# Kernel optimization log

Measured on AMD Instinct MI355X. Metric: run time of the kernel, lower is better.

## Reference

```python
import jax, jax.numpy as jnp
import numpy as np

L, H, C, HS, V, BS = 4, 8, 512, 64, 32000, 2048  # layers, heads, n_embd, head_size, vocab, block_size
B, T = 2, 2048


def _ln(x, g, b, eps=1e-5):
    m = jnp.mean(x, axis=-1, keepdims=True)
    v = jnp.var(x, axis=-1, keepdims=True)
    return (x - m) * jax.lax.rsqrt(v + eps) * g + b


def setup_inputs() -> dict:
    key = jax.random.key(0)
    ks = jax.random.split(key, 12)
    s = 0.02
    f = jnp.float32
    return {
        "idx": jax.random.randint(ks[0], (B, T), 0, V),
        "tok_emb": jax.random.normal(ks[1], (V, C), f) * s,
        "pos_emb": jax.random.normal(ks[2], (BS, C), f) * s,
        "ln1_g": jnp.ones((L, C), f), "ln1_b": jnp.zeros((L, C), f),
        "wq": jax.random.normal(ks[3], (L, H, C, HS), f) * s,
        "wk": jax.random.normal(ks[4], (L, H, C, HS), f) * s,
        "wv": jax.random.normal(ks[5], (L, H, C, HS), f) * s,
        "proj_w": jax.random.normal(ks[6], (L, C, C), f) * s,
        "proj_b": jnp.zeros((L, C), f),
        "ln2_g": jnp.ones((L, C), f), "ln2_b": jnp.zeros((L, C), f),
        "ff_w1": jax.random.normal(ks[7], (L, C, 4 * C), f) * s,
        "ff_b1": jnp.zeros((L, 4 * C), f),
        "ff_w2": jax.random.normal(ks[8], (L, 4 * C, C), f) * s,
        "ff_b2": jnp.zeros((L, C), f),
        "ffln_g": jnp.ones((L, C), f), "ffln_b": jnp.zeros((L, C), f),
        "lm_w": jax.random.normal(ks[9], (C, V), f) * s,
        "lm_b": jnp.zeros((V,), f),
    }


def reference(idx, tok_emb, pos_emb, ln1_g, ln1_b, wq, wk, wv, proj_w, proj_b,
              ln2_g, ln2_b, ff_w1, ff_b1, ff_w2, ff_b2, ffln_g, ffln_b, lm_w, lm_b):
    Tn = idx.shape[1]
    x = tok_emb[idx] + pos_emb[:Tn]  # [B,T,C]
    causal = jnp.tril(jnp.ones((Tn, Tn), bool))
    for l in range(L):
        h = _ln(x, ln1_g[l], ln1_b[l])
        q = jnp.einsum('btc,hcd->bhtd', h, wq[l])
        k = jnp.einsum('btc,hcd->bhtd', h, wk[l])
        v = jnp.einsum('btc,hcd->bhtd', h, wv[l])
        # NOTE: original module does NOT scale by 1/sqrt(head_size)
        wei = jnp.einsum('bhtd,bhsd->bhts', q, k)
        wei = jnp.where(causal, wei, -jnp.inf)
        wei = jax.nn.softmax(wei, axis=-1)
        att = jnp.einsum('bhts,bhsd->bhtd', wei, v)  # [B,H,T,HS]
        att = att.transpose(0, 2, 1, 3).reshape(x.shape[0], Tn, C)
        x = x + att @ proj_w[l].T + proj_b[l]
        h2 = _ln(x, ln2_g[l], ln2_b[l])
        ff = jax.nn.relu(h2 @ ff_w1[l] + ff_b1[l]) @ ff_w2[l] + ff_b2[l]
        ff = _ln(ff, ffln_g[l], ffln_b[l])  # FeedForward has trailing LayerNorm
        x = x + ff
    logits = x @ lm_w + lm_b  # [B,T,V]
    return logits
```

## Files before the change

### kernel.cpp

```cpp
#include <hip/hip_runtime.h>
#include <math.h>

#define NLAYER 4
#define NH     8
#define CDIM   512
#define HS     64
#define VOCAB  32000
#define BB     2
#define TT     2048
#define MROWS  (BB*TT)
#define QKVW   (3*CDIM)
#define NHEADS (BB*NH)
#define ASPLIT 2

typedef __attribute__((ext_vector_type(8))) short bf16x8;
typedef __attribute__((ext_vector_type(4))) float f32x4;

__device__ __forceinline__ unsigned short f2bf(float f) {
    unsigned int u = __float_as_uint(f);
    u += 0x7FFF + ((u >> 16) & 1);
    return (unsigned short)(u >> 16);
}

#define GLOAD16(g, l) __builtin_amdgcn_global_load_lds( \
    (const __attribute__((address_space(1))) void*)(g), \
    (__attribute__((address_space(3))) void*)(l), 16, 0, 0)

#define SWZ(row, chunk) (((row)*64) + ((((chunk) ^ ((row)&7)))*8))

template<int FLAGS, bool OUTBF, bool MSWIZ>
__global__ __launch_bounds__(256) void mfma_gemm(
    const unsigned short* __restrict__ A, int lda,
    const unsigned short* __restrict__ Bt, int ldb,
    const float* __restrict__ bias,
    void* __restrict__ Cout, int ldc,
    const float* __restrict__ resid,
    int K)
{
    __shared__ unsigned short As[2][128*64];
    __shared__ unsigned short Bs[2][128*64];
    const int tid = threadIdx.x;
    const int w = tid >> 6, l = tid & 63;
    const int wr = w >> 1, wc = w & 1;
    long m0, n0;
    if (MSWIZ) {
        const int mt = gridDim.x;
        const int flat = blockIdx.y * mt + blockIdx.x;
        const int cpx = (mt * gridDim.y) >> 3;
        const int swz = (flat & 7) * cpx + (flat >> 3);
        m0 = (long)(swz % mt) * 128;
        n0 = (long)(swz / mt) * 128;
    } else {
        m0 = (long)blockIdx.y * 128;
        n0 = (long)blockIdx.x * 128;
    }
    const int srow = l >> 3;
    const int scol = ((l & 7) ^ (srow & 7)) << 3;
    const unsigned short* Ab = A + m0*lda;
    const unsigned short* Bb = Bt + n0*ldb;
    const int fr = l & 15;
    const int g  = l >> 4;

    f32x4 acc[4][4];
    #pragma unroll
    for (int m = 0; m < 4; m++)
        #pragma unroll
        for (int n = 0; n < 4; n++) acc[m][n] = (f32x4)0.0f;

    auto stage = [&](int k0, int buf) {
        #pragma unroll
        for (int i = 0; i < 4; i++) {
            int seg = w*4 + i;
            GLOAD16(Ab + (long)(seg*8 + srow)*lda + k0 + scol, &As[buf][seg*512]);
            GLOAD16(Bb + (long)(seg*8 + srow)*ldb + k0 + scol, &Bs[buf][seg*512]);
        }
    };

    const int nk = K >> 6;
    stage(0, 0);
    for (int ks = 0; ks < nk; ks++) {
        const int buf = ks & 1;
        __syncthreads();
        if (ks + 1 < nk) stage((ks+1) << 6, buf ^ 1);
        #pragma unroll
        for (int kk = 0; kk < 2; kk++) {
            bf16x8 af[4], bf[4];
            #pragma unroll
            for (int m = 0; m < 4; m++) {
                int row = wr*64 + m*16 + fr;
                af[m] = *(const bf16x8*)&As[buf][SWZ(row, kk*4 + g)];
            }
            #pragma unroll
            for (int n = 0; n < 4; n++) {
                int row = wc*64 + n*16 + fr;
                bf[n] = *(const bf16x8*)&Bs[buf][SWZ(row, kk*4 + g)];
            }
            #pragma unroll
            for (int m = 0; m < 4; m++)
                #pragma unroll
                for (int n = 0; n < 4; n++)
                    acc[m][n] = __builtin_amdgcn_mfma_f32_16x16x32_bf16(
                        af[m], bf[n], acc[m][n], 0, 0, 0);
        }
    }

    const int rg = g << 2;
    #pragma unroll
    for (int n = 0; n < 4; n++) {
        long gn = n0 + wc*64 + n*16 + fr;
        float bv = (FLAGS & 1) ? bias[gn] : 0.f;
        #pragma unroll
        for (int m = 0; m < 4; m++) {
            #pragma unroll
            for (int r = 0; r < 4; r++) {
                long gm = m0 + wr*64 + m*16 + rg + r;
                float val = acc[m][n][r] + bv;
                if (FLAGS & 2) val = fmaxf(val, 0.f);
                if (FLAGS & 4) val += resid[gm*ldc + gn];
                if (OUTBF) {
                    ((unsigned short*)Cout)[gm*ldc + gn] = f2bf(val);
                } else if (FLAGS & 8) {
                    __builtin_nontemporal_store(val, &((float*)Cout)[gm*ldc + gn]);
                } else {
                    ((float*)Cout)[gm*ldc + gn] = val;
                }
            }
        }
    }
}

__global__ __launch_bounds__(256) void mfma_gemm_pk(
    const unsigned short* __restrict__ A, int lda,
    const unsigned short* __restrict__ Bt, int ldb,
    float* __restrict__ part, int ldc, long zstride,
    int Kc)
{
    __shared__ unsigned short As[2][128*64];
    __shared__ unsigned short Bs[2][128*64];
    const int tid = threadIdx.x;
    const int w = tid >> 6, l = tid & 63;
    const int wr = w >> 1, wc = w & 1;
    const long m0 = (long)blockIdx.y * 128;
    const long n0 = (long)blockIdx.x * 128;
    const int z = blockIdx.z;
    const int srow = l >> 3;
    const int scol = ((l & 7) ^ (srow & 7)) << 3;
    const unsigned short* Ab = A + m0*lda + (long)z*Kc;
    const unsigned short* Bb = Bt + n0*ldb + (long)z*Kc;
    float* Cb = part + (long)z*zstride;
    const int fr = l & 15;
    const int g  = l >> 4;

    f32x4 acc[4][4];
    #pragma unroll
    for (int m = 0; m < 4; m++)
        #pragma unroll
        for (int n = 0; n < 4; n++) acc[m][n] = (f32x4)0.0f;

    auto stage = [&](int k0, int buf) {
        #pragma unroll
        for (int i = 0; i < 4; i++) {
            int seg = w*4 + i;
            GLOAD16(Ab + (long)(seg*8 + srow)*lda + k0 + scol, &As[buf][seg*512]);
            GLOAD16(Bb + (long)(seg*8 + srow)*ldb + k0 + scol, &Bs[buf][seg*512]);
        }
    };

    const int nk = Kc >> 6;
    stage(0, 0);
    for (int ks = 0; ks < nk; ks++) {
        const int buf = ks & 1;
        __syncthreads();
        if (ks + 1 < nk) stage((ks+1) << 6, buf ^ 1);
        #pragma unroll
        for (int kk = 0; kk < 2; kk++) {
            bf16x8 af[4], bf[4];
            #pragma unroll
            for (int m = 0; m < 4; m++) {
                int row = wr*64 + m*16 + fr;
                af[m] = *(const bf16x8*)&As[buf][SWZ(row, kk*4 + g)];
            }
            #pragma unroll
            for (int n = 0; n < 4; n++) {
                int row = wc*64 + n*16 + fr;
                bf[n] = *(const bf16x8*)&Bs[buf][SWZ(row, kk*4 + g)];
            }
            #pragma unroll
            for (int m = 0; m < 4; m++)
                #pragma unroll
                for (int n = 0; n < 4; n++)
                    acc[m][n] = __builtin_amdgcn_mfma_f32_16x16x32_bf16(
                        af[m], bf[n], acc[m][n], 0, 0, 0);
        }
    }

    const int rg = g << 2;
    #pragma unroll
    for (int n = 0; n < 4; n++) {
        long gn = n0 + wc*64 + n*16 + fr;
        #pragma unroll
        for (int m = 0; m < 4; m++)
            #pragma unroll
            for (int r = 0; r < 4; r++) {
                long gm = m0 + wr*64 + m*16 + rg + r;
                Cb[gm*ldc + gn] = acc[m][n][r];
            }
    }
}

template<int NS, int RESID>
__global__ __launch_bounds__(256) void reduce_add(
    const float* __restrict__ part, const float* __restrict__ bias,
    float* __restrict__ out)
{
    const long i4 = ((long)blockIdx.x*256 + threadIdx.x) * 4;
    float4 s = *(const float4*)(bias + (i4 & (CDIM-1)));
    #pragma unroll
    for (int z = 0; z < NS; z++) {
        float4 p = *(const float4*)(part + (long)z*MROWS*CDIM + i4);
        s.x += p.x; s.y += p.y; s.z += p.z; s.w += p.w;
    }
    float4* o = (float4*)(out + i4);
    if (RESID) {
        float4 old = *o;
        s.x += old.x; s.y += old.y; s.z += old.z; s.w += old.w;
    }
    *o = s;
}

__global__ __launch_bounds__(256) void mfma_gemm_qkv(
    const unsigned short* __restrict__ A,
    const unsigned short* __restrict__ Bt,
    unsigned short* __restrict__ qh,
    unsigned short* __restrict__ kh,
    unsigned short* __restrict__ vt)
{
    __shared__ unsigned short As[2][128*64];
    __shared__ unsigned short Bs[2][128*64];
    const int tid = threadIdx.x;
    const int w = tid >> 6, l = tid & 63;
    const int wr = w >> 1, wc = w & 1;
    const long m0 = (long)blockIdx.y * 128;
    const long n0 = (long)blockIdx.x * 128;
    const int srow = l >> 3;
    const int scol = ((l & 7) ^ (srow & 7)) << 3;
    const unsigned short* Ab = A + m0*CDIM;
    const unsigned short* Bb = Bt + n0*CDIM;
    const int fr = l & 15;
    const int g  = l >> 4;

    f32x4 acc[4][4];
    #pragma unroll
    for (int m = 0; m < 4; m++)
        #pragma unroll
        for (int n = 0; n < 4; n++) acc[m][n] = (f32x4)0.0f;

    auto stage = [&](int k0, int buf) {
        #pragma unroll
        for (int i = 0; i < 4; i++) {
            int seg = w*4 + i;
            GLOAD16(Ab + (long)(seg*8 + srow)*CDIM + k0 + scol, &As[buf][seg*512]);
            GLOAD16(Bb + (long)(seg*8 + srow)*CDIM + k0 + scol, &Bs[buf][seg*512]);
        }
    };

    const int nk = CDIM >> 6;
    stage(0, 0);
    for (int ks = 0; ks < nk; ks++) {
        const int buf = ks & 1;
        __syncthreads();
        if (ks + 1 < nk) stage((ks+1) << 6, buf ^ 1);
        #pragma unroll
        for (int kk = 0; kk < 2; kk++) {
            bf16x8 af[4], bf[4];
            #pragma unroll
            for (int m = 0; m < 4; m++) {
                int row = wr*64 + m*16 + fr;
                af[m] = *(const bf16x8*)&As[buf][SWZ(row, kk*4 + g)];
            }
            #pragma unroll
            for (int n = 0; n < 4; n++) {
                int row = wc*64 + n*16 + fr;
                bf[n] = *(const bf16x8*)&Bs[buf][SWZ(row, kk*4 + g)];
            }
            #pragma unroll
            for (int m = 0; m < 4; m++)
                #pragma unroll
                for (int n = 0; n < 4; n++)
                    acc[m][n] = __builtin_amdgcn_mfma_f32_16x16x32_bf16(
                        af[m], bf[n], acc[m][n], 0, 0, 0);
        }
    }

    const int rg = g << 2;
    #pragma unroll
    for (int n = 0; n < 4; n++) {
        int gn = (int)(n0 + wc*64 + n*16 + fr);
        int which = gn >> 9, hh = (gn >> 6) & 7, d = gn & 63;
        #pragma unroll
        for (int m = 0; m < 4; m++) {
            #pragma unroll
            for (int r = 0; r < 4; r++) {
                int gm = (int)(m0 + wr*64 + m*16 + rg + r);
                int b = gm >> 11, t = gm & (TT-1);
                int head = b*NH + hh;
                unsigned short val = f2bf(acc[m][n][r]);
                if (which == 0)      qh[((long)head*TT + t)*HS + d] = val;
                else if (which == 1) kh[((long)head*TT + t)*HS + d] = val;
                else                 vt[((long)head*HS + d)*TT + t] = val;
            }
        }
    }
}

__global__ __launch_bounds__(256) void attn_part(
    const unsigned short* __restrict__ qh,
    const unsigned short* __restrict__ kh,
    const unsigned short* __restrict__ vt,
    float* __restrict__ oP, float* __restrict__ ml)
{
    __shared__ unsigned short Ks[2][64*64];
    __shared__ unsigned short Vts[2][64*64];
    __shared__ unsigned short Ps[4][32*72];
    const int tid = threadIdx.x;
    const int w = tid >> 6, l = tid & 63;
    const int fr = l & 15, g = l >> 4;
    const int head = blockIdx.y;
    const int sp = blockIdx.z;
    const int x = blockIdx.x;
    const int qw = x*128 + w*32;
    const unsigned short* Qb = qh + (long)head*TT*HS;
    const unsigned short* Kb = kh + (long)head*TT*HS;
    const unsigned short* Vb = vt + (long)head*HS*TT;

    bf16x8 aq[2][2];
    #pragma unroll
    for (int mt = 0; mt < 2; mt++)
        #pragma unroll
        for (int ks = 0; ks < 2; ks++)
            aq[mt][ks] = *(const bf16x8*)&Qb[(long)(qw + mt*16 + fr)*HS + ks*32 + g*8];

    f32x4 acc_o[2][4];
    float mrun[2][4], lsum[2][4];
    #pragma unroll
    for (int mt = 0; mt < 2; mt++) {
        #pragma unroll
        for (int r = 0; r < 4; r++) { mrun[mt][r] = -INFINITY; lsum[mt][r] = 0.f; }
        #pragma unroll
        for (int n = 0; n < 4; n++) acc_o[mt][n] = (f32x4)0.0f;
    }

    const int nch = 2*x + 2;
    const int qq = nch / ASPLIT, rr = nch % ASPLIT;
    const int cbeg = sp*qq + (sp < rr ? sp : rr);
    const int cend = cbeg + qq + (sp < rr ? 1 : 0);
    const int srow = l >> 3;
    const int scol = ((l & 7) ^ (srow & 7)) << 3;

    auto stage = [&](int c) {
        int buf = c & 1;
        int s0_ = c*64;
        #pragma unroll
        for (int i = 0; i < 2; i++) {
            int rb = i*32 + w*8;
            GLOAD16(Kb + (long)(s0_ + rb + srow)*HS + scol, &Ks[buf][rb*64]);
            GLOAD16(Vb + (long)(rb + srow)*TT + s0_ + scol, &Vts[buf][rb*64]);
        }
    };

    if (cbeg < cend) stage(cbeg);
    for (int c = cbeg; c < cend; c++) {
        const int s0 = c*64;
        const int buf = c & 1;
        __syncthreads();
        if (c + 1 < cend) stage(c+1);
        if (s0 > qw + 31) continue;

        bf16x8 bk[4][2];
        #pragma unroll
        for (int n = 0; n < 4; n++)
            #pragma unroll
            for (int ks = 0; ks < 2; ks++) {
                int row = n*16 + fr;
                bk[n][ks] = *(const bf16x8*)&Ks[buf][SWZ(row, ks*4 + g)];
            }
        f32x4 sc[2][4];
        #pragma unroll
        for (int mt = 0; mt < 2; mt++)
            #pragma unroll
            for (int n = 0; n < 4; n++) sc[mt][n] = (f32x4)0.0f;
        #pragma unroll
        for (int ks = 0; ks < 2; ks++)
            #pragma unroll
            for (int mt = 0; mt < 2; mt++)
                #pragma unroll
                for (int n = 0; n < 4; n++)
                    sc[mt][n] = __builtin_amdgcn_mfma_f32_16x16x32_bf16(
                        aq[mt][ks], bk[n][ks], sc[mt][n], 0, 0, 0);

        #pragma unroll
        for (int mt = 0; mt < 2; mt++) {
            #pragma unroll
            for (int r = 0; r < 4; r++) {
                int q = qw + mt*16 + g*4 + r;
                float rmax = -INFINITY;
                #pragma unroll
                for (int n = 0; n < 4; n++) {
                    float v = sc[mt][n][r];
                    v = (s0 + n*16 + fr <= q) ? v : -INFINITY;
                    sc[mt][n][r] = v;
                    rmax = fmaxf(rmax, v);
                }
                #pragma unroll
                for (int off = 8; off >= 1; off >>= 1)
                    rmax = fmaxf(rmax, __shfl_xor(rmax, off));
                float mnew = fmaxf(mrun[mt][r], rmax);
                float scale = __expf(mrun[mt][r] - mnew);
                float ps = 0.f;
                #pragma unroll
                for (int n = 0; n < 4; n++) {
                    float p = __expf(sc[mt][n][r] - mnew);
                    sc[mt][n][r] = p;
                    ps += p;
                }
                #pragma unroll
                for (int off = 8; off >= 1; off >>= 1)
                    ps += __shfl_xor(ps, off);
                lsum[mt][r] = lsum[mt][r]*scale + ps;
                mrun[mt][r] = mnew;
                #pragma unroll
                for (int n = 0; n < 4; n++) acc_o[mt][n][r] *= scale;
            }
        }

        #pragma unroll
        for (int mt = 0; mt < 2; mt++)
            #pragma unroll
            for (int n = 0; n < 4; n++)
                #pragma unroll
                for (int r = 0; r < 4; r++)
                    Ps[w][(mt*16 + g*4 + r)*72 + n*16 + fr] = f2bf(sc[mt][n][r]);

        bf16x8 ap[2][2], bv[4][2];
        #pragma unroll
        for (int mt = 0; mt < 2; mt++)
            #pragma unroll
            for (int ks = 0; ks < 2; ks++)
                ap[mt][ks] = *(const bf16x8*)&Ps[w][(mt*16 + fr)*72 + ks*32 + g*8];
        #pragma unroll
        for (int n = 0; n < 4; n++)
            #pragma unroll
            for (int ks = 0; ks < 2; ks++) {
                int row = n*16 + fr;
                bv[n][ks] = *(const bf16x8*)&Vts[buf][SWZ(row, ks*4 + g)];
            }
        #pragma unroll
        for (int ks = 0; ks < 2; ks++)
            #pragma unroll
            for (int mt = 0; mt < 2; mt++)
                #pragma unroll
                for (int n = 0; n < 4; n++)
                    acc_o[mt][n] = __builtin_amdgcn_mfma_f32_16x16x32_bf16(
                        ap[mt][ks], bv[n][ks], acc_o[mt][n], 0, 0, 0);
    }

    float* oB = oP + ((long)(head*ASPLIT + sp)*TT)*HS;
    float* mlB = ml + ((long)(head*ASPLIT + sp)*TT)*2;
    #pragma unroll
    for (int mt = 0; mt < 2; mt++) {
        #pragma unroll
        for (int n = 0; n < 4; n++)
            #pragma unroll
            for (int r = 0; r < 4; r++)
                oB[(long)(qw + mt*16 + g*4 + r)*HS + n*16 + fr] = acc_o[mt][n][r];
        if (fr == 0) {
            #pragma unroll
            for (int r = 0; r < 4; r++) {
                int t = qw + mt*16 + g*4 + r;
                mlB[t*2]     = mrun[mt][r];
                mlB[t*2 + 1] = lsum[mt][r];
            }
        }
    }
}

__global__ __launch_bounds__(256) void attn_combine(
    const float* __restrict__ oP, const float* __restrict__ ml,
    unsigned short* __restrict__ att)
{
    const int gid = blockIdx.x*4 + (threadIdx.x >> 6);
    const int lane = threadIdx.x & 63;
    const int head = gid >> 11, t = gid & (TT-1);
    const int b = head >> 3, hh = head & 7;
    float m[ASPLIT], lv[ASPLIT];
    float M = -INFINITY;
    #pragma unroll
    for (int s = 0; s < ASPLIT; s++) {
        long i = (long)(head*ASPLIT + s)*TT + t;
        m[s] = ml[i*2]; lv[s] = ml[i*2+1];
        M = fmaxf(M, m[s]);
    }
    float L = 0.f, v = 0.f;
    #pragma unroll
    for (int s = 0; s < ASPLIT; s++) {
        float e = __expf(m[s] - M);
        L += lv[s]*e;
        v += oP[((long)(head*ASPLIT + s)*TT + t)*HS + lane]*e;
    }
    att[((long)b*TT + t)*CDIM + hh*HS + lane] = f2bf(v / L);
}

__global__ __launch_bounds__(256) void transpose_cast(
    const float* __restrict__ in, unsigned short* __restrict__ out,
    int R, int Cn, long in_z1, long in_z2, long out_z1, long out_z2, int z2n)
{
    const int z = blockIdx.z;
    const int z1 = z / z2n, z2 = z % z2n;
    const float* ip = in + (long)z1*in_z1 + (long)z2*in_z2;
    unsigned short* op = out + (long)z1*out_z1 + (long)z2*out_z2;
    __shared__ float tile[32][33];
    const int tx = threadIdx.x & 31, ty = threadIdx.x >> 5;
    const long r0 = (long)blockIdx.y*32, c0 = (long)blockIdx.x*32;
    #pragma unroll
    for (int i = 0; i < 4; i++)
        tile[ty + i*8][tx] = ip[(r0 + ty + i*8)*Cn + c0 + tx];
    __syncthreads();
    #pragma unroll
    for (int i = 0; i < 4; i++)
        op[(c0 + ty + i*8)*R + r0 + tx] = f2bf(tile[tx][ty + i*8]);
}

__global__ __launch_bounds__(256) void cast_kernel(
    const float* __restrict__ in, unsigned short* __restrict__ out, long n)
{
    long i = ((long)blockIdx.x*256 + threadIdx.x) * 4;
    if (i >= n) return;
    float4 v = *(const float4*)(in + i);
    ushort4 u = make_ushort4(f2bf(v.x), f2bf(v.y), f2bf(v.z), f2bf(v.w));
    *(ushort4*)(out + i) = u;
}

__global__ void embed_kernel(const int* __restrict__ idx,
                             const float* __restrict__ tok,
                             const float* __restrict__ pos,
                             float* __restrict__ x)
{
    const int r = blockIdx.x;
    const int t = r & (TT-1);
    const long tr = idx[r];
    const float* te = tok + tr*CDIM;
    const float* pe = pos + (long)t*CDIM;
    float* xo = x + (long)r*CDIM;
    for (int c = threadIdx.x; c < CDIM; c += blockDim.x)
        xo[c] = te[c] + pe[c];
}

template<int MODE>
__global__ __launch_bounds__(256) void ln_kernel(
    const float* __restrict__ in, const float* __restrict__ g,
    const float* __restrict__ bb, void* __restrict__ outp,
    void* __restrict__ outp2)
{
    const int wave = threadIdx.x >> 6;
    const int lane = threadIdx.x & 63;
    const long r = (long)blockIdx.x*4 + wave;
    const float* xr = in + r*CDIM;
    float vals[8];
    float s = 0.f;
    #pragma unroll
    for (int i = 0; i < 8; i++) { vals[i] = xr[lane + i*64]; s += vals[i]; }
    #pragma unroll
    for (int o = 32; o >= 1; o >>= 1) s += __shfl_xor(s, o);
    const float mean = s * (1.f/CDIM);
    float vs = 0.f;
    #pragma unroll
    for (int i = 0; i < 8; i++) { float d = vals[i]-mean; vs += d*d; }
    #pragma unroll
    for (int o = 32; o >= 1; o >>= 1) vs += __shfl_xor(vs, o);
    const float rstd = rsqrtf(vs*(1.f/CDIM) + 1e-5f);
    #pragma unroll
    for (int i = 0; i < 8; i++) {
        int c = lane + i*64;
        float nv = (vals[i]-mean)*rstd*g[c] + bb[c];
        if (MODE == 1) {
            ((unsigned short*)outp)[r*CDIM + c] = f2bf(nv);
        } else {
            float s2 = ((float*)outp)[r*CDIM + c] + nv;
            ((float*)outp)[r*CDIM + c] = s2;
            if (MODE == 3) ((unsigned short*)outp2)[r*CDIM + c] = f2bf(s2);
        }
    }
}

extern "C" void kernel_launch(void* const* d_in, const int* in_sizes, int n_in,
                              void* d_out, int out_size, void* d_ws, size_t ws_size,
                              hipStream_t stream)
{
    const int*   idx   = (const int*)  d_in[0];
    const float* tok   = (const float*)d_in[1];
    const float* pos   = (const float*)d_in[2];
    const float* ln1g  = (const float*)d_in[3];
    const float* ln1b  = (const float*)d_in[4];
    const float* wq    = (const float*)d_in[5];
    const float* wk    = (const float*)d_in[6];
    const float* wv    = (const float*)d_in[7];
    const float* projw = (const float*)d_in[8];
    const float* projb = (const float*)d_in[9];
    const float* ln2g  = (const float*)d_in[10];
    const float* ln2b  = (const float*)d_in[11];
    const float* ffw1  = (const float*)d_in[12];
    const float* ffb1  = (const float*)d_in[13];
    const float* ffw2  = (const float*)d_in[14];
    const float* ffb2  = (const float*)d_in[15];
    const float* flng  = (const float*)d_in[16];
    const float* flnb  = (const float*)d_in[17];
    const float* lmw   = (const float*)d_in[18];
    const float* lmb   = (const float*)d_in[19];
    float* out = (float*)d_out;

    char* wp = (char*)d_ws;
    float* x  = (float*)wp;           wp += (size_t)MROWS*CDIM*4;
    float* ff = (float*)wp;           wp += (size_t)MROWS*CDIM*4;
    unsigned short* h     = (unsigned short*)wp; wp += (size_t)MROWS*CDIM*2;
    unsigned short* lmt   = (unsigned short*)wp; wp += (size_t)VOCAB*CDIM*2;
    unsigned short* ff1t  = (unsigned short*)wp; wp += (size_t)NLAYER*4*CDIM*CDIM*2;
    unsigned short* ff2t  = (unsigned short*)wp; wp += (size_t)NLAYER*4*CDIM*CDIM*2;
    unsigned short* qkvt  = (unsigned short*)wp; wp += (size_t)NLAYER*QKVW*CDIM*2;
    unsigned short* projc = (unsigned short*)wp; wp += (size_t)NLAYER*CDIM*CDIM*2;
    unsigned short* qh    = (unsigned short*)wp; wp += (size_t)NHEADS*TT*HS*2;
    unsigned short* kh    = (unsigned short*)wp; wp += (size_t)NHEADS*TT*HS*2;
    unsigned short* vt    = (unsigned short*)wp; wp += (size_t)NHEADS*TT*HS*2;

    unsigned short* f1  = (unsigned short*)d_out;
    unsigned short* att = f1 + (size_t)MROWS*4*CDIM;
    float* oP = (float*)(att + (size_t)MROWS*CDIM);
    float* ml = oP + (size_t)NHEADS*ASPLIT*TT*HS;
    float* pP = ml + (size_t)NHEADS*ASPLIT*TT*2;
    float* fP = pP + (size_t)2*MROWS*CDIM;

    transpose_cast<<<dim3(VOCAB/32, CDIM/32, 1), 256, 0, stream>>>(
        lmw, lmt, CDIM, VOCAB, 0, 0, 0, 0, 1);
    transpose_cast<<<dim3(4*CDIM/32, CDIM/32, NLAYER), 256, 0, stream>>>(
        ffw1, ff1t, CDIM, 4*CDIM, (long)CDIM*4*CDIM, 0, (long)4*CDIM*CDIM, 0, 1);
    transpose_cast<<<dim3(CDIM/32, 4*CDIM/32, NLAYER), 256, 0, stream>>>(
        ffw2, ff2t, 4*CDIM, CDIM, (long)4*CDIM*CDIM, 0, (long)CDIM*4*CDIM, 0, 1);
    {
        const size_t QBLK = (size_t)CDIM * CDIM;
        transpose_cast<<<dim3(HS/32, CDIM/32, NLAYER*NH), 256, 0, stream>>>(
            wq, qkvt,            CDIM, HS,
            (long)NH*CDIM*HS, (long)CDIM*HS, (long)QKVW*CDIM, (long)HS*CDIM, NH);
        transpose_cast<<<dim3(HS/32, CDIM/32, NLAYER*NH), 256, 0, stream>>>(
            wk, qkvt + QBLK,     CDIM, HS,
            (long)NH*CDIM*HS, (long)CDIM*HS, (long)QKVW*CDIM, (long)HS*CDIM, NH);
        transpose_cast<<<dim3(HS/32, CDIM/32, NLAYER*NH), 256, 0, stream>>>(
            wv, qkvt + 2*QBLK,   CDIM, HS,
            (long)NH*CDIM*HS, (long)CDIM*HS, (long)QKVW*CDIM, (long)HS*CDIM, NH);
    }
    cast_kernel<<<(NLAYER*CDIM*CDIM/4 + 255)/256, 256, 0, stream>>>(
        projw, projc, (long)NLAYER*CDIM*CDIM);

    embed_kernel<<<MROWS, 256, 0, stream>>>(idx, tok, pos, x);

    const int RBLK = (MROWS*CDIM/4) / 256;

    for (int l = 0; l < NLAYER; l++) {
        const unsigned short* qkvt_l = qkvt + (size_t)l*QKVW*CDIM;
        const unsigned short* projc_l = projc + (size_t)l*CDIM*CDIM;
        const unsigned short* ff1t_l = ff1t + (size_t)l*4*CDIM*CDIM;
        const unsigned short* ff2t_l = ff2t + (size_t)l*4*CDIM*CDIM;

        ln_kernel<1><<<MROWS/4, 256, 0, stream>>>(x, ln1g + l*CDIM, ln1b + l*CDIM, h, nullptr);

        mfma_gemm_qkv<<<dim3(QKVW/128, MROWS/128), 256, 0, stream>>>(
            h, qkvt_l, qh, kh, vt);

        attn_part<<<dim3(TT/128, NHEADS, ASPLIT), 256, 0, stream>>>(qh, kh, vt, oP, ml);
        attn_combine<<<dim3(NHEADS*TT/4), 256, 0, stream>>>(oP, ml, att);

        mfma_gemm_pk<<<dim3(CDIM/128, MROWS/128, 2), 256, 0, stream>>>(
            att, CDIM, projc_l, CDIM, pP, CDIM, (long)MROWS*CDIM, 256);
        reduce_add<2,1><<<RBLK, 256, 0, stream>>>(pP, projb + l*CDIM, x);

        ln_kernel<1><<<MROWS/4, 256, 0, stream>>>(x, ln2g + l*CDIM, ln2b + l*CDIM, h, nullptr);

        mfma_gemm<3,true,false><<<dim3(4*CDIM/128, MROWS/128), 256, 0, stream>>>(
            h, CDIM, ff1t_l, CDIM, ffb1 + (size_t)l*4*CDIM, f1, 4*CDIM, nullptr, CDIM);

        mfma_gemm_pk<<<dim3(CDIM/128, MROWS/128, 4), 256, 0, stream>>>(
            f1, 4*CDIM, ff2t_l, 4*CDIM, fP, CDIM, (long)MROWS*CDIM, 512);
        reduce_add<4,0><<<RBLK, 256, 0, stream>>>(fP, ffb2 + l*CDIM, ff);

        if (l == NLAYER-1)
            ln_kernel<3><<<MROWS/4, 256, 0, stream>>>(ff, flng + l*CDIM, flnb + l*CDIM, x, h);
        else
            ln_kernel<2><<<MROWS/4, 256, 0, stream>>>(ff, flng + l*CDIM, flnb + l*CDIM, x, nullptr);
    }

    mfma_gemm<9,false,true><<<dim3(MROWS/128, VOCAB/128), 256, 0, stream>>>(
        h, CDIM, lmt, CDIM, lmb, out, VOCAB, nullptr, CDIM);
}
```

Measured before the change: 1.004 ms.

## Drop split-K for proj/FF2 GEMMs and use 256x256 tiles for LM head

The projection and FF2 GEMMs no longer use split-K with separate reduce kernels. A single GEMM now fuses the bias, and for the projection the residual add, into its epilogue. This removes the partial-sum buffers and two launches per layer, but halves or quarters the grid, so these GEMMs launch only 128 blocks. The LM-head GEMM moves to a new 512-thread kernel with 256x256 tiles and a swizzled block order, and drops the nontemporal store, aiming for more operand reuse per LDS load at the cost of 128KB LDS per block and lower occupancy.

```diff
diff --git a/kernel.cpp b/kernel.cpp
--- a/kernel.cpp
+++ b/kernel.cpp
@@ -28,7 +28,7 @@
 
 #define SWZ(row, chunk) (((row)*64) + ((((chunk) ^ ((row)&7)))*8))
 
-template<int FLAGS, bool OUTBF, bool MSWIZ>
+template<int FLAGS, bool OUTBF>
 __global__ __launch_bounds__(256) void mfma_gemm(
     const unsigned short* __restrict__ A, int lda,
     const unsigned short* __restrict__ Bt, int ldb,
@@ -42,18 +42,8 @@
     const int tid = threadIdx.x;
     const int w = tid >> 6, l = tid & 63;
     const int wr = w >> 1, wc = w & 1;
-    long m0, n0;
-    if (MSWIZ) {
-        const int mt = gridDim.x;
-        const int flat = blockIdx.y * mt + blockIdx.x;
-        const int cpx = (mt * gridDim.y) >> 3;
-        const int swz = (flat & 7) * cpx + (flat >> 3);
-        m0 = (long)(swz % mt) * 128;
-        n0 = (long)(swz / mt) * 128;
-    } else {
-        m0 = (long)blockIdx.y * 128;
-        n0 = (long)blockIdx.x * 128;
-    }
+    const long m0 = (long)blockIdx.y * 128;
+    const long n0 = (long)blockIdx.x * 128;
     const int srow = l >> 3;
     const int scol = ((l & 7) ^ (srow & 7)) << 3;
     const unsigned short* Ab = A + m0*lda;
@@ -117,43 +107,41 @@
                 float val = acc[m][n][r] + bv;
                 if (FLAGS & 2) val = fmaxf(val, 0.f);
                 if (FLAGS & 4) val += resid[gm*ldc + gn];
-                if (OUTBF) {
-                    ((unsigned short*)Cout)[gm*ldc + gn] = f2bf(val);
-                } else if (FLAGS & 8) {
-                    __builtin_nontemporal_store(val, &((float*)Cout)[gm*ldc + gn]);
-                } else {
-                    ((float*)Cout)[gm*ldc + gn] = val;
-                }
-            }
-        }
-    }
-}
-
-__global__ __launch_bounds__(256) void mfma_gemm_pk(
+                if (OUTBF) ((unsigned short*)Cout)[gm*ldc + gn] = f2bf(val);
+                else       ((float*)Cout)[gm*ldc + gn] = val;
+            }
+        }
+    }
+}
+
+__global__ __launch_bounds__(512, 2) void mfma_gemm_256(
     const unsigned short* __restrict__ A, int lda,
     const unsigned short* __restrict__ Bt, int ldb,
-    float* __restrict__ part, int ldc, long zstride,
-    int Kc)
-{
-    __shared__ unsigned short As[2][128*64];
-    __shared__ unsigned short Bs[2][128*64];
+    const float* __restrict__ bias,
+    float* __restrict__ Cout, int ldc,
+    int K)
+{
+    __shared__ unsigned short As[2][256*64];
+    __shared__ unsigned short Bs[2][256*64];
     const int tid = threadIdx.x;
     const int w = tid >> 6, l = tid & 63;
-    const int wr = w >> 1, wc = w & 1;
-    const long m0 = (long)blockIdx.y * 128;
-    const long n0 = (long)blockIdx.x * 128;
-    const int z = blockIdx.z;
+    const int wr = w >> 2, wc = w & 3;
+    const int mt = gridDim.x;
+    const int flat = blockIdx.y * mt + blockIdx.x;
+    const int cpx = (mt * gridDim.y) >> 3;
+    const int swz = (flat & 7) * cpx + (flat >> 3);
+    const long m0 = (long)(swz % mt) * 256;
+    const long n0 = (long)(swz / mt) * 256;
     const int srow = l >> 3;
     const int scol = ((l & 7) ^ (srow & 7)) << 3;
-    const unsigned short* Ab = A + m0*lda + (long)z*Kc;
-    const unsigned short* Bb = Bt + n0*ldb + (long)z*Kc;
-    float* Cb = part + (long)z*zstride;
+    const unsigned short* Ab = A + m0*lda;
+    const unsigned short* Bb = Bt + n0*ldb;
     const int fr = l & 15;
     const int g  = l >> 4;
 
-    f32x4 acc[4][4];
-    #pragma unroll
-    for (int m = 0; m < 4; m++)
+    f32x4 acc[8][4];
+    #pragma unroll
+    for (int m = 0; m < 8; m++)
         #pragma unroll
         for (int n = 0; n < 4; n++) acc[m][n] = (f32x4)0.0f;
 
@@ -166,7 +154,7 @@
         }
     };
 
-    const int nk = Kc >> 6;
+    const int nk = K >> 6;
     stage(0, 0);
     for (int ks = 0; ks < nk; ks++) {
         const int buf = ks & 1;
@@ -174,23 +162,21 @@
         if (ks + 1 < nk) stage((ks+1) << 6, buf ^ 1);
         #pragma unroll
         for (int kk = 0; kk < 2; kk++) {
-            bf16x8 af[4], bf[4];
-            #pragma unroll
-            for (int m = 0; m < 4; m++) {
-                int row = wr*64 + m*16 + fr;
-                af[m] = *(const bf16x8*)&As[buf][SWZ(row, kk*4 + g)];
-            }
+            bf16x8 bf[4];
             #pragma unroll
             for (int n = 0; n < 4; n++) {
                 int row = wc*64 + n*16 + fr;
                 bf[n] = *(const bf16x8*)&Bs[buf][SWZ(row, kk*4 + g)];
             }
             #pragma unroll
-            for (int m = 0; m < 4; m++)
+            for (int m = 0; m < 8; m++) {
+                int row = wr*128 + m*16 + fr;
+                bf16x8 af = *(const bf16x8*)&As[buf][SWZ(row, kk*4 + g)];
                 #pragma unroll
                 for (int n = 0; n < 4; n++)
                     acc[m][n] = __builtin_amdgcn_mfma_f32_16x16x32_bf16(
-                        af[m], bf[n], acc[m][n], 0, 0, 0);
+                        af, bf[n], acc[m][n], 0, 0, 0);
+            }
         }
     }
 
@@ -198,34 +184,16 @@
     #pragma unroll
     for (int n = 0; n < 4; n++) {
         long gn = n0 + wc*64 + n*16 + fr;
-        #pragma unroll
-        for (int m = 0; m < 4; m++)
+        float bv = bias[gn];
+        #pragma unroll
+        for (int m = 0; m < 8; m++) {
             #pragma unroll
             for (int r = 0; r < 4; r++) {
-                long gm = m0 + wr*64 + m*16 + rg + r;
-                Cb[gm*ldc + gn] = acc[m][n][r];
-            }
-    }
-}
-
-template<int NS, int RESID>
-__global__ __launch_bounds__(256) void reduce_add(
-    const float* __restrict__ part, const float* __restrict__ bias,
-    float* __restrict__ out)
-{
-    const long i4 = ((long)blockIdx.x*256 + threadIdx.x) * 4;
-    float4 s = *(const float4*)(bias + (i4 & (CDIM-1)));
-    #pragma unroll
-    for (int z = 0; z < NS; z++) {
-        float4 p = *(const float4*)(part + (long)z*MROWS*CDIM + i4);
-        s.x += p.x; s.y += p.y; s.z += p.z; s.w += p.w;
-    }
-    float4* o = (float4*)(out + i4);
-    if (RESID) {
-        float4 old = *o;
-        s.x += old.x; s.y += old.y; s.z += old.z; s.w += old.w;
-    }
-    *o = s;
+                long gm = m0 + wr*128 + m*16 + rg + r;
+                Cout[gm*ldc + gn] = acc[m][n][r] + bv;
+            }
+        }
+    }
 }
 
 __global__ __launch_bounds__(256) void mfma_gemm_qkv(
@@ -635,8 +603,6 @@
     unsigned short* att = f1 + (size_t)MROWS*4*CDIM;
     float* oP = (float*)(att + (size_t)MROWS*CDIM);
     float* ml = oP + (size_t)NHEADS*ASPLIT*TT*HS;
-    float* pP = ml + (size_t)NHEADS*ASPLIT*TT*2;
-    float* fP = pP + (size_t)2*MROWS*CDIM;
 
     transpose_cast<<<dim3(VOCAB/32, CDIM/32, 1), 256, 0, stream>>>(
         lmw, lmt, CDIM, VOCAB, 0, 0, 0, 0, 1);
@@ -661,8 +627,6 @@
 
     embed_kernel<<<MROWS, 256, 0, stream>>>(idx, tok, pos, x);
 
-    const int RBLK = (MROWS*CDIM/4) / 256;
-
     for (int l = 0; l < NLAYER; l++) {
         const unsigned short* qkvt_l = qkvt + (size_t)l*QKVW*CDIM;
         const unsigned short* projc_l = projc + (size_t)l*CDIM*CDIM;
@@ -677,18 +641,16 @@
         attn_part<<<dim3(TT/128, NHEADS, ASPLIT), 256, 0, stream>>>(qh, kh, vt, oP, ml);
         attn_combine<<<dim3(NHEADS*TT/4), 256, 0, stream>>>(oP, ml, att);
 
-        mfma_gemm_pk<<<dim3(CDIM/128, MROWS/128, 2), 256, 0, stream>>>(
-            att, CDIM, projc_l, CDIM, pP, CDIM, (long)MROWS*CDIM, 256);
-        reduce_add<2,1><<<RBLK, 256, 0, stream>>>(pP, projb + l*CDIM, x);
+        mfma_gemm<5,false><<<dim3(CDIM/128, MROWS/128), 256, 0, stream>>>(
+            att, CDIM, projc_l, CDIM, projb + l*CDIM, x, CDIM, x, CDIM);
 
         ln_kernel<1><<<MROWS/4, 256, 0, stream>>>(x, ln2g + l*CDIM, ln2b + l*CDIM, h, nullptr);
 
-        mfma_gemm<3,true,false><<<dim3(4*CDIM/128, MROWS/128), 256, 0, stream>>>(
+        mfma_gemm<3,true><<<dim3(4*CDIM/128, MROWS/128), 256, 0, stream>>>(
             h, CDIM, ff1t_l, CDIM, ffb1 + (size_t)l*4*CDIM, f1, 4*CDIM, nullptr, CDIM);
 
-        mfma_gemm_pk<<<dim3(CDIM/128, MROWS/128, 4), 256, 0, stream>>>(
-            f1, 4*CDIM, ff2t_l, 4*CDIM, fP, CDIM, (long)MROWS*CDIM, 512);
-        reduce_add<4,0><<<RBLK, 256, 0, stream>>>(fP, ffb2 + l*CDIM, ff);
+        mfma_gemm<1,false><<<dim3(CDIM/128, MROWS/128), 256, 0, stream>>>(
+            f1, 4*CDIM, ff2t_l, 4*CDIM, ffb2 + l*CDIM, ff, CDIM, nullptr, 4*CDIM);
 
         if (l == NLAYER-1)
             ln_kernel<3><<<MROWS/4, 256, 0, stream>>>(ff, flng + l*CDIM, flnb + l*CDIM, x, h);
@@ -696,6 +658,6 @@
             ln_kernel<2><<<MROWS/4, 256, 0, stream>>>(ff, flng + l*CDIM, flnb + l*CDIM, x, nullptr);
     }
 
-    mfma_gemm<9,false,true><<<dim3(MROWS/128, VOCAB/128), 256, 0, stream>>>(
-        h, CDIM, lmt, CDIM, lmb, out, VOCAB, nullptr, CDIM);
-}
+    mfma_gemm_256<<<dim3(MROWS/256, VOCAB/256), 512, 0, stream>>>(
+        h, CDIM, lmt, CDIM, lmb, out, VOCAB, CDIM);
+}
```

New measurement: 1.002 ms. Within noise of the previous version (-0.2%).
